# Performance work log

Measured on AMD Instinct MI355X. Metric: run time of the kernel, lower is better.

Reference implementation:

```python
import jax, jax.numpy as jnp
import numpy as np

NUM_CLASSES = 10
MAX_V = 81  # max_width * max_height = 9*9


def _ln(x, w, eps=1e-5):
    # torch LayerNorm with bias=False (weight only)
    m = jnp.mean(x, axis=-1, keepdims=True)
    v = jnp.var(x, axis=-1, keepdims=True)
    return (x - m) / jnp.sqrt(v + eps) * w


def _mha(q_in, k_in, v_in, in_proj, out_proj, nhead):
    # torch nn.MultiheadAttention, bias=False
    d = q_in.shape[-1]
    Wq, Wk, Wv = in_proj[:d], in_proj[d:2 * d], in_proj[2 * d:]
    q = q_in @ Wq.T
    k = k_in @ Wk.T
    v = v_in @ Wv.T
    B, Lq, _ = q.shape
    Lk = k.shape[1]
    hd = d // nhead
    q = q.reshape(B, Lq, nhead, hd)
    k = k.reshape(B, Lk, nhead, hd)
    v = v.reshape(B, Lk, nhead, hd)
    scores = jnp.einsum('bqhd,bkhd->bhqk', q, k) / jnp.sqrt(jnp.asarray(hd, q.dtype))
    attn = jax.nn.softmax(scores, axis=-1)
    o = jnp.einsum('bhqk,bkhd->bqhd', attn, v).reshape(B, Lq, d)
    return o @ out_proj.T


def setup_inputs() -> dict:
    key = jax.random.key(0)
    ks = jax.random.split(key, 16)
    N, C, H, W = 16, NUM_CLASSES, 30, 30
    d = C + 1  # 11
    V = 32

    def rn(k, shape, s=0.2):
        return (jax.random.normal(k, shape) * s).astype(jnp.float32)

    return {
        'x': jax.random.normal(ks[0], (N, C, H, W), dtype=jnp.float32),
        'V_feature': rn(ks[1], (C, V), 1.0),
        'enc_in_proj': rn(ks[2], (3 * d, d)),
        'enc_out_proj': rn(ks[3], (d, d)),
        'enc_lin1': rn(ks[4], (1, d)),
        'enc_lin2': rn(ks[5], (d, 1)),
        'enc_ln1': jnp.ones((d,), jnp.float32),
        'enc_ln2': jnp.ones((d,), jnp.float32),
        'ffV_w': rn(ks[6], (V, MAX_V)),
        'dec_sa_in': rn(ks[7], (3 * V, V)),
        'dec_sa_out': rn(ks[8], (V, V)),
        'dec_ca_in': rn(ks[9], (3 * V, V)),
        'dec_ca_out': rn(ks[10], (V, V)),
        'dec_lin1': rn(ks[11], (1, V)),
        'dec_lin2': rn(ks[12], (V, 1)),
        'dec_ln1': jnp.ones((V,), jnp.float32),
        'dec_ln2': jnp.ones((V,), jnp.float32),
        'dec_ln3': jnp.ones((V,), jnp.float32),
        'W_d0': rn(ks[13], (8, V)),
        'W_d1': rn(ks[14], (1, 8)),
    }


def reference(x, V_feature, enc_in_proj, enc_out_proj, enc_lin1, enc_lin2,
              enc_ln1, enc_ln2, ffV_w, dec_sa_in, dec_sa_out, dec_ca_in,
              dec_ca_out, dec_lin1, dec_lin2, dec_ln1, dec_ln2, dec_ln3,
              W_d0, W_d1):
    N, C, H, W = x.shape
    # PixelVectorExtractor: pad(0) + all-ones channel padded with 1, 3x3 unfold
    xp = jnp.pad(x, ((0, 0), (0, 0), (1, 1), (1, 1)))
    ones = jnp.ones((N, 1, H + 2, W + 2), x.dtype)
    xc = jnp.concatenate([xp, ones], axis=1)  # [N, C+1, H+2, W+2]
    # row-major 3x3 patch order matches torch unfold(0,3,1).unfold(1,3,1)
    patches = jnp.stack([xc[:, :, di:di + H, dj:dj + W]
                         for di in range(3) for dj in range(3)], axis=-1)
    feat = patches.transpose(0, 2, 3, 1, 4).reshape(N * H * W, C + 1, 9)
    feat = jnp.pad(feat, ((0, 0), (0, 0), (0, MAX_V - 9)))  # [B, C+1, 81]

    # TransformerEncoder (1 layer, post-norm, nhead=1, relu FF, no dropout)
    f = feat.transpose(0, 2, 1)  # [B, 81, C+1]
    f = _ln(f + _mha(f, f, f, enc_in_proj, enc_out_proj, 1), enc_ln1)
    f = _ln(f + jax.nn.relu(f @ enc_lin1.T) @ enc_lin2.T, enc_ln2)
    f = f.transpose(0, 2, 1)  # [B, C+1, 81]

    mem = f @ ffV_w.T  # ff_V: Linear(81 -> 32, no bias) -> [B, C+1, 32]
    B, _, V = mem.shape

    # TransformerDecoder (1 layer, post-norm, nhead=32 so head_dim=1)
    y = jnp.broadcast_to(V_feature, (B, C, V))
    y = _ln(y + _mha(y, y, y, dec_sa_in, dec_sa_out, V), dec_ln1)
    y = _ln(y + _mha(y, mem, mem, dec_ca_in, dec_ca_out, V), dec_ln2)
    y = _ln(y + jax.nn.relu(y @ dec_lin1.T) @ dec_lin2.T, dec_ln3)

    # decode MLP: 32 -> 8 -> 1
    y = jax.nn.relu(y @ W_d0.T) @ W_d1.T  # [B, C, 1]
    return y.reshape(N, H, W, C).transpose(0, 3, 1, 2)
```

## Files before the change

### kernel.cpp

```cpp
#include <hip/hip_runtime.h>
#include <math.h>


__device__ __forceinline__ float gsum32(float v) {
#pragma unroll
  for (int m = 16; m > 0; m >>= 1) v += __shfl_xor(v, m, 32);
  return v;
}

__global__ __launch_bounds__(256) void precompute_kernel(
    const float* __restrict__ Vf,
    const float* __restrict__ enc_in,
    const float* __restrict__ enc_outw,
    const float* __restrict__ ffV_w,
    const float* __restrict__ dec_sa_in,
    const float* __restrict__ dec_sa_out,
    const float* __restrict__ dec_ln1,
    const float* __restrict__ dec_ca_in,
    float* __restrict__ M_enc, float* __restrict__ WVO,
    float* __restrict__ G_k, float* __restrict__ G_v,
    float* __restrict__ y1, float* __restrict__ qca)
{
  const int tid = threadIdx.x;
  const float rs11 = 0.3015113445777636f;

  for (int idx = tid; idx < 121; idx += 256) {
    int c = idx / 11, cp = idx - c * 11;
    float sm = 0.f, sv = 0.f;
    for (int i = 0; i < 11; ++i) {
      sm += enc_in[i * 11 + c] * enc_in[(11 + i) * 11 + cp];
      sv += enc_outw[c * 11 + i] * enc_in[(22 + i) * 11 + cp];
    }
    M_enc[idx] = sm * rs11;
    WVO[idx] = sv;
  }

  __shared__ float Fsh[320];
  for (int idx = tid; idx < 288; idx += 256) {
    int t = idx >> 5, j = idx & 31;
    Fsh[idx] = ffV_w[j * 81 + t];
  }
  if (tid < 32) {
    float s = 0.f;
    for (int t = 9; t < 81; ++t) s += ffV_w[tid * 81 + t];
    Fsh[288 + tid] = s;
  }
  __syncthreads();

  for (int idx = tid; idx < 640; idx += 256) {
    int which = idx >= 320;
    int r = idx - 320 * which;
    int t = r >> 5, h = r & 31;
    const float* w = dec_ca_in + ((which ? 64 : 32) + h) * 32;
    float s = 0.f;
    for (int j = 0; j < 32; ++j) s += Fsh[t * 32 + j] * w[j];
    (which ? G_v : G_k)[r] = s;
  }

  __shared__ float qsa[320], ksa[320], vsa[320], osa[320], zb[320];
  __shared__ float mu[16], rstd[16];

  for (int idx = tid; idx < 960; idx += 256) {
    int m = idx / 320, r = idx - m * 320;
    int t = r >> 5, h = r & 31;
    const float* w = dec_sa_in + (m * 32 + h) * 32;
    const float* yr = Vf + t * 32;
    float s = 0.f;
#pragma unroll
    for (int j = 0; j < 32; ++j) s += yr[j] * w[j];
    (m == 0 ? qsa : m == 1 ? ksa : vsa)[r] = s;
  }
  __syncthreads();

  for (int idx = tid; idx < 320; idx += 256) {
    int h = idx & 31;
    float q = qsa[idx];
    float sc[10];
    float mx = -1e30f;
#pragma unroll
    for (int s = 0; s < 10; ++s) { sc[s] = q * ksa[s * 32 + h]; mx = fmaxf(mx, sc[s]); }
    float den = 0.f, acc = 0.f;
#pragma unroll
    for (int s = 0; s < 10; ++s) {
      float e = __expf(sc[s] - mx);
      den += e;
      acc += e * vsa[s * 32 + h];
    }
    osa[idx] = acc / den;
  }
  __syncthreads();

  for (int idx = tid; idx < 320; idx += 256) {
    int t = idx >> 5, c = idx & 31;
    float s = 0.f;
#pragma unroll
    for (int h = 0; h < 32; ++h) s += osa[t * 32 + h] * dec_sa_out[c * 32 + h];
    zb[idx] = Vf[idx] + s;
  }
  __syncthreads();

  if (tid < 10) {
    float s1 = 0.f, s2 = 0.f;
    for (int c = 0; c < 32; ++c) { float z = zb[tid * 32 + c]; s1 += z; s2 += z * z; }
    float m = s1 * (1.f / 32.f);
    mu[tid] = m;
    rstd[tid] = 1.f / sqrtf(s2 * (1.f / 32.f) - m * m + 1e-5f);
  }
  __syncthreads();

  for (int idx = tid; idx < 320; idx += 256) {
    int t = idx >> 5, c = idx & 31;
    float v = (zb[idx] - mu[t]) * rstd[t] * dec_ln1[c];
    y1[idx] = v;
    zb[idx] = v;
  }
  __syncthreads();

  for (int idx = tid; idx < 320; idx += 256) {
    int t = idx >> 5, h = idx & 31;
    const float* w = dec_ca_in + h * 32;
    float s = 0.f;
#pragma unroll
    for (int j = 0; j < 32; ++j) s += zb[t * 32 + j] * w[j];
    qca[idx] = s;
  }
}

#define SLICE 1376

__global__ __launch_bounds__(256) void pixel_main_kernel(
    const float* __restrict__ x,
    const float* __restrict__ M_enc, const float* __restrict__ WVO,
    const float* __restrict__ enc_lin1, const float* __restrict__ enc_lin2,
    const float* __restrict__ enc_ln1, const float* __restrict__ enc_ln2,
    const float* __restrict__ G_k, const float* __restrict__ G_v,
    const float* __restrict__ y1g, const float* __restrict__ qcag,
    const float* __restrict__ dec_ca_out,
    const float* __restrict__ dec_lin1, const float* __restrict__ dec_lin2,
    const float* __restrict__ dec_ln2v, const float* __restrict__ dec_ln3v,
    const float* __restrict__ W_d0, const float* __restrict__ W_d1,
    float* __restrict__ out)
{
  __shared__ __align__(16) float sh[4 * SLICE];
  const int wave = threadIdx.x >> 6;
  const int lane = threadIdx.x & 63;
  float* ls = sh + wave * SLICE;
  const int F9 = 0, G = 112, VO = 224, SC = 336, ZR = 432, FE = 544, KC = 656, VC = 1008;
  const int OC = 0, ZB = 320;

  for (int pp = 0; pp < 2; ++pp) {
    const int p = blockIdx.x * 8 + pp * 4 + wave;
    const int n = p / 900;
    const int rem = p - n * 900;
    const int pi = rem / 30, pj = rem - (rem / 30) * 30;

    for (int idx = lane; idx < 99; idx += 64) {
      int t = idx / 11, c = idx - t * 11;
      float val = 1.0f;
      if (c < 10) {
        int di = t / 3, dj = t - (t / 3) * 3;
        int ii = pi + di - 1, jj = pj + dj - 1;
        val = (ii >= 0 && ii < 30 && jj >= 0 && jj < 30)
                  ? x[((n * 10 + c) * 30 + ii) * 30 + jj] : 0.0f;
      }
      ls[F9 + idx] = val;
    }
    __syncthreads();

    for (int idx = lane; idx < 99; idx += 64) {
      int s = idx / 11, c = idx - (idx / 11) * 11;
      const float* Mr = M_enc + c * 11;
      const float* Wr = WVO + c * 11;
      float ag = 0.f, av = 0.f;
#pragma unroll
      for (int cp = 0; cp < 11; ++cp) {
        float fv = ls[F9 + s * 11 + cp];
        ag += Mr[cp] * fv;
        av += Wr[cp] * fv;
      }
      ls[G + idx] = ag;
      ls[VO + idx] = av;
    }
    __syncthreads();

    for (int idx = lane; idx < 81; idx += 64) {
      int t = idx / 9, s = idx - t * 9;
      float a = 0.f;
#pragma unroll
      for (int c = 0; c < 11; ++c) a += ls[F9 + t * 11 + c] * ls[G + s * 11 + c];
      ls[SC + idx] = a;
    }
    __syncthreads();

    if (lane < 9) {
      float m = 0.f;
#pragma unroll
      for (int s = 0; s < 9; ++s) m = fmaxf(m, ls[SC + lane * 9 + s]);
      ls[FE + lane] = m;
    }
    __syncthreads();

    for (int idx = lane; idx < 81; idx += 64) {
      int t = idx / 9;
      ls[SC + idx] = __expf(ls[SC + idx] - ls[FE + t]);
    }
    __syncthreads();

    if (lane < 9) {
      float den = 72.0f * __expf(-ls[FE + lane]);
#pragma unroll
      for (int s = 0; s < 9; ++s) den += ls[SC + lane * 9 + s];
      ls[FE + 16 + lane] = 1.0f / den;
    }
    __syncthreads();

    for (int idx = lane; idx < 110; idx += 64) {
      int t = idx / 11, c = idx - t * 11;
      float a = 0.f;
      if (t < 9) {
#pragma unroll
        for (int s = 0; s < 9; ++s) a += ls[SC + t * 9 + s] * ls[VO + s * 11 + c];
        a = a * ls[FE + 16 + t] + ls[F9 + idx];
      } else {
#pragma unroll
        for (int s = 0; s < 9; ++s) a += ls[VO + s * 11 + c];
        a *= (1.0f / 81.0f);
      }
      ls[ZR + idx] = a;
    }
    __syncthreads();

    if (lane < 10) {
      float s1 = 0.f, s2 = 0.f;
#pragma unroll
      for (int c = 0; c < 11; ++c) { float z = ls[ZR + lane * 11 + c]; s1 += z; s2 += z * z; }
      float m = s1 * (1.0f / 11.0f);
      ls[SC + lane] = m;
      ls[SC + 16 + lane] = 1.0f / sqrtf(s2 * (1.0f / 11.0f) - m * m + 1e-5f);
    }
    __syncthreads();

    for (int idx = lane; idx < 110; idx += 64) {
      int t = idx / 11, c = idx - t * 11;
      ls[ZR + idx] = (ls[ZR + idx] - ls[SC + t]) * ls[SC + 16 + t] * enc_ln1[c];
    }
    __syncthreads();

    if (lane < 10) {
      float h = 0.f;
#pragma unroll
      for (int c = 0; c < 11; ++c) h += ls[ZR + lane * 11 + c] * enc_lin1[c];
      h = fmaxf(h, 0.f);
      float s1 = 0.f, s2 = 0.f;
#pragma unroll
      for (int c = 0; c < 11; ++c) {
        float z = ls[ZR + lane * 11 + c] + h * enc_lin2[c];
        s1 += z; s2 += z * z;
      }
      float m = s1 * (1.0f / 11.0f);
      ls[SC + 32 + lane] = h;
      ls[SC + 48 + lane] = m;
      ls[SC + 64 + lane] = 1.0f / sqrtf(s2 * (1.0f / 11.0f) - m * m + 1e-5f);
    }
    __syncthreads();

    for (int idx = lane; idx < 110; idx += 64) {
      int t = idx / 11, c = idx - t * 11;
      float z = ls[ZR + idx] + ls[SC + 32 + t] * enc_lin2[c];
      ls[FE + idx] = (z - ls[SC + 48 + t]) * ls[SC + 64 + t] * enc_ln2[c];
    }
    __syncthreads();

    {
      const int h = lane & 31, grp = lane >> 5;
      const float* Gb = grp ? G_v : G_k;
      const int dst = grp ? VC : KC;
      float gr[10];
#pragma unroll
      for (int t = 0; t < 10; ++t) gr[t] = Gb[t * 32 + h];
#pragma unroll
      for (int c = 0; c < 11; ++c) {
        float a = 0.f;
#pragma unroll
        for (int t = 0; t < 10; ++t) a += ls[FE + t * 11 + c] * gr[t];
        ls[dst + c * 32 + h] = a;
      }
    }
    __syncthreads();

    for (int it = 0; it < 5; ++it) {
      int idx = it * 64 + lane;
      int t = idx >> 5, h = idx & 31;
      float q = qcag[t * 32 + h];
      float kreg[11];
#pragma unroll
      for (int s = 0; s < 11; ++s) kreg[s] = q * ls[KC + s * 32 + h];
      float mx = kreg[0];
#pragma unroll
      for (int s = 1; s < 11; ++s) mx = fmaxf(mx, kreg[s]);
      float den = 0.f, acc = 0.f;
#pragma unroll
      for (int s = 0; s < 11; ++s) {
        float e = __expf(kreg[s] - mx);
        den += e;
        acc += e * ls[VC + s * 32 + h];
      }
      ls[OC + idx] = acc / den;
    }
    __syncthreads();

    for (int k = 0; k < 5; ++k) {
      int t = 2 * k + (lane >> 5);
      int c = lane & 31;
      float zacc = 0.f;
      const float4* wrow = (const float4*)(dec_ca_out + c * 32);
      const float4* orow = (const float4*)(ls + OC + t * 32);
#pragma unroll
      for (int h4 = 0; h4 < 8; ++h4) {
        float4 o4 = orow[h4];
        float4 w4 = wrow[h4];
        zacc += o4.x * w4.x + o4.y * w4.y + o4.z * w4.z + o4.w * w4.w;
      }
      float z = y1g[t * 32 + c] + zacc;
      {
        float s1 = gsum32(z), s2 = gsum32(z * z);
        float mu = s1 * (1.0f / 32.0f);
        z = (z - mu) * (1.0f / sqrtf(s2 * (1.0f / 32.0f) - mu * mu + 1e-5f)) * dec_ln2v[c];
      }
      {
        float d1 = gsum32(z * dec_lin1[c]);
        z += fmaxf(d1, 0.f) * dec_lin2[c];
      }
      {
        float s1 = gsum32(z), s2 = gsum32(z * z);
        float mu = s1 * (1.0f / 32.0f);
        z = (z - mu) * (1.0f / sqrtf(s2 * (1.0f / 32.0f) - mu * mu + 1e-5f)) * dec_ln3v[c];
      }
      ls[ZB + t * 32 + c] = z;
    }
    __syncthreads();

    for (int idx = lane; idx < 80; idx += 64) {
      int t = idx >> 3, m = idx & 7;
      const float4* arow = (const float4*)(W_d0 + m * 32);
      const float4* zrow4 = (const float4*)(ls + ZB + t * 32);
      float d = 0.f;
#pragma unroll
      for (int q4 = 0; q4 < 8; ++q4) {
        float4 a4 = arow[q4];
        float4 z4 = zrow4[q4];
        d += a4.x * z4.x + a4.y * z4.y + a4.z * z4.z + a4.w * z4.w;
      }
      ls[OC + idx] = fmaxf(d, 0.f);
    }
    __syncthreads();

    if (lane < 10) {
      float r = 0.f;
#pragma unroll
      for (int m = 0; m < 8; ++m) r += ls[OC + lane * 8 + m] * W_d1[m];
      out[((n * 10 + lane) * 30 + pi) * 30 + pj] = r;
    }
    __syncthreads();
  }
}

extern "C" void kernel_launch(void* const* d_in, const int* in_sizes, int n_in,
                              void* d_out, int out_size, void* d_ws, size_t ws_size,
                              hipStream_t stream) {
  (void)in_sizes; (void)n_in; (void)out_size; (void)ws_size;
  const float* x          = (const float*)d_in[0];
  const float* Vf         = (const float*)d_in[1];
  const float* enc_in     = (const float*)d_in[2];
  const float* enc_outw   = (const float*)d_in[3];
  const float* enc_lin1   = (const float*)d_in[4];
  const float* enc_lin2   = (const float*)d_in[5];
  const float* enc_ln1    = (const float*)d_in[6];
  const float* enc_ln2    = (const float*)d_in[7];
  const float* ffV_w      = (const float*)d_in[8];
  const float* dec_sa_in  = (const float*)d_in[9];
  const float* dec_sa_out = (const float*)d_in[10];
  const float* dec_ca_in  = (const float*)d_in[11];
  const float* dec_ca_out = (const float*)d_in[12];
  const float* dec_lin1   = (const float*)d_in[13];
  const float* dec_lin2   = (const float*)d_in[14];
  const float* dec_ln1    = (const float*)d_in[15];
  const float* dec_ln2    = (const float*)d_in[16];
  const float* dec_ln3    = (const float*)d_in[17];
  const float* W_d0       = (const float*)d_in[18];
  const float* W_d1       = (const float*)d_in[19];
  float* out = (float*)d_out;

  float* ws    = (float*)d_ws;
  float* M_enc = ws;
  float* WVO   = ws + 128;
  float* G_k   = ws + 256;
  float* G_v   = ws + 576;
  float* y1    = ws + 896;
  float* qca   = ws + 1216;

  hipLaunchKernelGGL(precompute_kernel, dim3(1), dim3(256), 0, stream,
                     Vf, enc_in, enc_outw, ffV_w, dec_sa_in, dec_sa_out,
                     dec_ln1, dec_ca_in, M_enc, WVO, G_k, G_v, y1, qca);

  hipLaunchKernelGGL(pixel_main_kernel, dim3(1800), dim3(256), 0, stream,
                     x, M_enc, WVO, enc_lin1, enc_lin2, enc_ln1, enc_ln2,
                     G_k, G_v, y1, qca, dec_ca_out, dec_lin1, dec_lin2,
                     dec_ln2, dec_ln3, W_d0, W_d1, out);
}
```

Measured before the change: 202.6 us.

## Replace block barriers with per-wave LDS waits, split precompute, one pixel per wave

```diff
diff --git a/kernel.cpp b/kernel.cpp
--- a/kernel.cpp
+++ b/kernel.cpp
@@ -6,6 +6,10 @@
 #pragma unroll
   for (int m = 16; m > 0; m >>= 1) v += __shfl_xor(v, m, 32);
   return v;
+}
+
+__device__ __forceinline__ void wsync() {
+  asm volatile("s_waitcnt lgkmcnt(0)" ::: "memory");
 }
 
 __global__ __launch_bounds__(256) void precompute_kernel(
@@ -22,107 +26,109 @@
     float* __restrict__ y1, float* __restrict__ qca)
 {
   const int tid = threadIdx.x;
-  const float rs11 = 0.3015113445777636f;
-
-  for (int idx = tid; idx < 121; idx += 256) {
-    int c = idx / 11, cp = idx - c * 11;
-    float sm = 0.f, sv = 0.f;
-    for (int i = 0; i < 11; ++i) {
-      sm += enc_in[i * 11 + c] * enc_in[(11 + i) * 11 + cp];
-      sv += enc_outw[c * 11 + i] * enc_in[(22 + i) * 11 + cp];
-    }
-    M_enc[idx] = sm * rs11;
-    WVO[idx] = sv;
-  }
-
-  __shared__ float Fsh[320];
-  for (int idx = tid; idx < 288; idx += 256) {
-    int t = idx >> 5, j = idx & 31;
-    Fsh[idx] = ffV_w[j * 81 + t];
-  }
-  if (tid < 32) {
-    float s = 0.f;
-    for (int t = 9; t < 81; ++t) s += ffV_w[tid * 81 + t];
-    Fsh[288 + tid] = s;
-  }
-  __syncthreads();
-
-  for (int idx = tid; idx < 640; idx += 256) {
-    int which = idx >= 320;
-    int r = idx - 320 * which;
-    int t = r >> 5, h = r & 31;
-    const float* w = dec_ca_in + ((which ? 64 : 32) + h) * 32;
-    float s = 0.f;
-    for (int j = 0; j < 32; ++j) s += Fsh[t * 32 + j] * w[j];
-    (which ? G_v : G_k)[r] = s;
-  }
-
-  __shared__ float qsa[320], ksa[320], vsa[320], osa[320], zb[320];
-  __shared__ float mu[16], rstd[16];
-
-  for (int idx = tid; idx < 960; idx += 256) {
-    int m = idx / 320, r = idx - m * 320;
-    int t = r >> 5, h = r & 31;
-    const float* w = dec_sa_in + (m * 32 + h) * 32;
-    const float* yr = Vf + t * 32;
-    float s = 0.f;
-#pragma unroll
-    for (int j = 0; j < 32; ++j) s += yr[j] * w[j];
-    (m == 0 ? qsa : m == 1 ? ksa : vsa)[r] = s;
-  }
-  __syncthreads();
-
-  for (int idx = tid; idx < 320; idx += 256) {
-    int h = idx & 31;
-    float q = qsa[idx];
-    float sc[10];
-    float mx = -1e30f;
-#pragma unroll
-    for (int s = 0; s < 10; ++s) { sc[s] = q * ksa[s * 32 + h]; mx = fmaxf(mx, sc[s]); }
-    float den = 0.f, acc = 0.f;
-#pragma unroll
-    for (int s = 0; s < 10; ++s) {
-      float e = __expf(sc[s] - mx);
-      den += e;
-      acc += e * vsa[s * 32 + h];
-    }
-    osa[idx] = acc / den;
-  }
-  __syncthreads();
-
-  for (int idx = tid; idx < 320; idx += 256) {
-    int t = idx >> 5, c = idx & 31;
-    float s = 0.f;
-#pragma unroll
-    for (int h = 0; h < 32; ++h) s += osa[t * 32 + h] * dec_sa_out[c * 32 + h];
-    zb[idx] = Vf[idx] + s;
-  }
-  __syncthreads();
-
-  if (tid < 10) {
-    float s1 = 0.f, s2 = 0.f;
-    for (int c = 0; c < 32; ++c) { float z = zb[tid * 32 + c]; s1 += z; s2 += z * z; }
-    float m = s1 * (1.f / 32.f);
-    mu[tid] = m;
-    rstd[tid] = 1.f / sqrtf(s2 * (1.f / 32.f) - m * m + 1e-5f);
-  }
-  __syncthreads();
-
-  for (int idx = tid; idx < 320; idx += 256) {
-    int t = idx >> 5, c = idx & 31;
-    float v = (zb[idx] - mu[t]) * rstd[t] * dec_ln1[c];
-    y1[idx] = v;
-    zb[idx] = v;
-  }
-  __syncthreads();
-
-  for (int idx = tid; idx < 320; idx += 256) {
-    int t = idx >> 5, h = idx & 31;
-    const float* w = dec_ca_in + h * 32;
-    float s = 0.f;
-#pragma unroll
-    for (int j = 0; j < 32; ++j) s += zb[t * 32 + j] * w[j];
-    qca[idx] = s;
+
+  if (blockIdx.x == 0) {
+    const float rs11 = 0.3015113445777636f;
+    for (int idx = tid; idx < 121; idx += 256) {
+      int c = idx / 11, cp = idx - c * 11;
+      float sm = 0.f, sv = 0.f;
+      for (int i = 0; i < 11; ++i) {
+        sm += enc_in[i * 11 + c] * enc_in[(11 + i) * 11 + cp];
+        sv += enc_outw[c * 11 + i] * enc_in[(22 + i) * 11 + cp];
+      }
+      M_enc[idx] = sm * rs11;
+      WVO[idx] = sv;
+    }
+
+    __shared__ float Fsh[320];
+    for (int idx = tid; idx < 288; idx += 256) {
+      int t = idx >> 5, j = idx & 31;
+      Fsh[idx] = ffV_w[j * 81 + t];
+    }
+    if (tid < 32) {
+      float s = 0.f;
+      for (int t = 9; t < 81; ++t) s += ffV_w[tid * 81 + t];
+      Fsh[288 + tid] = s;
+    }
+    __syncthreads();
+
+    for (int idx = tid; idx < 640; idx += 256) {
+      int which = idx >= 320;
+      int r = idx - 320 * which;
+      int t = r >> 5, h = r & 31;
+      const float* w = dec_ca_in + ((which ? 64 : 32) + h) * 32;
+      float s = 0.f;
+      for (int j = 0; j < 32; ++j) s += Fsh[t * 32 + j] * w[j];
+      (which ? G_v : G_k)[r] = s;
+    }
+  } else {
+    __shared__ float qsa[320], ksa[320], vsa[320], osa[320], zb[320];
+    __shared__ float mu[16], rstd[16];
+
+    for (int idx = tid; idx < 960; idx += 256) {
+      int m = idx / 320, r = idx - m * 320;
+      int t = r >> 5, h = r & 31;
+      const float* w = dec_sa_in + (m * 32 + h) * 32;
+      const float* yr = Vf + t * 32;
+      float s = 0.f;
+#pragma unroll
+      for (int j = 0; j < 32; ++j) s += yr[j] * w[j];
+      (m == 0 ? qsa : m == 1 ? ksa : vsa)[r] = s;
+    }
+    __syncthreads();
+
+    for (int idx = tid; idx < 320; idx += 256) {
+      int h = idx & 31;
+      float q = qsa[idx];
+      float sc[10];
+      float mx = -1e30f;
+#pragma unroll
+      for (int s = 0; s < 10; ++s) { sc[s] = q * ksa[s * 32 + h]; mx = fmaxf(mx, sc[s]); }
+      float den = 0.f, acc = 0.f;
+#pragma unroll
+      for (int s = 0; s < 10; ++s) {
+        float e = __expf(sc[s] - mx);
+        den += e;
+        acc += e * vsa[s * 32 + h];
+      }
+      osa[idx] = acc / den;
+    }
+    __syncthreads();
+
+    for (int idx = tid; idx < 320; idx += 256) {
+      int t = idx >> 5, c = idx & 31;
+      float s = 0.f;
+#pragma unroll
+      for (int h = 0; h < 32; ++h) s += osa[t * 32 + h] * dec_sa_out[c * 32 + h];
+      zb[idx] = Vf[idx] + s;
+    }
+    __syncthreads();
+
+    if (tid < 10) {
+      float s1 = 0.f, s2 = 0.f;
+      for (int c = 0; c < 32; ++c) { float z = zb[tid * 32 + c]; s1 += z; s2 += z * z; }
+      float m = s1 * (1.f / 32.f);
+      mu[tid] = m;
+      rstd[tid] = 1.f / sqrtf(s2 * (1.f / 32.f) - m * m + 1e-5f);
+    }
+    __syncthreads();
+
+    for (int idx = tid; idx < 320; idx += 256) {
+      int t = idx >> 5, c = idx & 31;
+      float v = (zb[idx] - mu[t]) * rstd[t] * dec_ln1[c];
+      y1[idx] = v;
+      zb[idx] = v;
+    }
+    __syncthreads();
+
+    for (int idx = tid; idx < 320; idx += 256) {
+      int t = idx >> 5, h = idx & 31;
+      const float* w = dec_ca_in + h * 32;
+      float s = 0.f;
+#pragma unroll
+      for (int j = 0; j < 32; ++j) s += zb[t * 32 + j] * w[j];
+      qca[idx] = s;
+    }
   }
 }
 
@@ -148,220 +154,200 @@
   const int F9 = 0, G = 112, VO = 224, SC = 336, ZR = 432, FE = 544, KC = 656, VC = 1008;
   const int OC = 0, ZB = 320;
 
-  for (int pp = 0; pp < 2; ++pp) {
-    const int p = blockIdx.x * 8 + pp * 4 + wave;
-    const int n = p / 900;
-    const int rem = p - n * 900;
-    const int pi = rem / 30, pj = rem - (rem / 30) * 30;
-
-    for (int idx = lane; idx < 99; idx += 64) {
-      int t = idx / 11, c = idx - t * 11;
-      float val = 1.0f;
-      if (c < 10) {
-        int di = t / 3, dj = t - (t / 3) * 3;
-        int ii = pi + di - 1, jj = pj + dj - 1;
-        val = (ii >= 0 && ii < 30 && jj >= 0 && jj < 30)
-                  ? x[((n * 10 + c) * 30 + ii) * 30 + jj] : 0.0f;
-      }
-      ls[F9 + idx] = val;
-    }
-    __syncthreads();
-
-    for (int idx = lane; idx < 99; idx += 64) {
-      int s = idx / 11, c = idx - (idx / 11) * 11;
-      const float* Mr = M_enc + c * 11;
-      const float* Wr = WVO + c * 11;
-      float ag = 0.f, av = 0.f;
-#pragma unroll
-      for (int cp = 0; cp < 11; ++cp) {
-        float fv = ls[F9 + s * 11 + cp];
-        ag += Mr[cp] * fv;
-        av += Wr[cp] * fv;
-      }
-      ls[G + idx] = ag;
-      ls[VO + idx] = av;
-    }
-    __syncthreads();
-
-    for (int idx = lane; idx < 81; idx += 64) {
-      int t = idx / 9, s = idx - t * 9;
+  const int p = blockIdx.x * 4 + wave;
+  const int n = p / 900;
+  const int rem = p - n * 900;
+  const int pi = rem / 30, pj = rem - (rem / 30) * 30;
+
+  for (int idx = lane; idx < 99; idx += 64) {
+    int t = idx / 11, c = idx - t * 11;
+    float val = 1.0f;
+    if (c < 10) {
+      int di = t / 3, dj = t - (t / 3) * 3;
+      int ii = pi + di - 1, jj = pj + dj - 1;
+      val = (ii >= 0 && ii < 30 && jj >= 0 && jj < 30)
+                ? x[((n * 10 + c) * 30 + ii) * 30 + jj] : 0.0f;
+    }
+    ls[F9 + idx] = val;
+  }
+  wsync();
+
+  for (int idx = lane; idx < 99; idx += 64) {
+    int s = idx / 11, c = idx - (idx / 11) * 11;
+    const float* Mr = M_enc + c * 11;
+    const float* Wr = WVO + c * 11;
+    float ag = 0.f, av = 0.f;
+#pragma unroll
+    for (int cp = 0; cp < 11; ++cp) {
+      float fv = ls[F9 + s * 11 + cp];
+      ag += Mr[cp] * fv;
+      av += Wr[cp] * fv;
+    }
+    ls[G + idx] = ag;
+    ls[VO + idx] = av;
+  }
+  wsync();
+
+  for (int idx = lane; idx < 81; idx += 64) {
+    int t = idx / 9, s = idx - (idx / 9) * 9;
+    float a = 0.f;
+#pragma unroll
+    for (int c = 0; c < 11; ++c) a += ls[F9 + t * 11 + c] * ls[G + s * 11 + c];
+    ls[SC + idx] = a;
+  }
+  wsync();
+
+  if (lane < 9) {
+    float e[9];
+    float mx = 0.0f;
+#pragma unroll
+    for (int s = 0; s < 9; ++s) { e[s] = ls[SC + lane * 9 + s]; mx = fmaxf(mx, e[s]); }
+    float den = 72.0f * __expf(-mx);
+#pragma unroll
+    for (int s = 0; s < 9; ++s) {
+      e[s] = __expf(e[s] - mx);
+      den += e[s];
+      ls[SC + lane * 9 + s] = e[s];
+    }
+    ls[SC + 81 + lane] = 1.0f / den;
+  }
+  wsync();
+
+  for (int idx = lane; idx < 110; idx += 64) {
+    int t = idx / 11, c = idx - (idx / 11) * 11;
+    float a = 0.f;
+    if (t < 9) {
+#pragma unroll
+      for (int s = 0; s < 9; ++s) a += ls[SC + t * 9 + s] * ls[VO + s * 11 + c];
+      a = a * ls[SC + 81 + t] + ls[F9 + idx];
+    } else {
+#pragma unroll
+      for (int s = 0; s < 9; ++s) a += ls[VO + s * 11 + c];
+      a *= (1.0f / 81.0f);
+    }
+    ls[ZR + idx] = a;
+  }
+  wsync();
+
+  if (lane < 10) {
+    float row[11];
+#pragma unroll
+    for (int c = 0; c < 11; ++c) row[c] = ls[ZR + lane * 11 + c];
+    float s1 = 0.f, s2 = 0.f;
+#pragma unroll
+    for (int c = 0; c < 11; ++c) { s1 += row[c]; s2 += row[c] * row[c]; }
+    float mu = s1 * (1.0f / 11.0f);
+    float rs = 1.0f / sqrtf(s2 * (1.0f / 11.0f) - mu * mu + 1e-5f);
+    float h = 0.f;
+#pragma unroll
+    for (int c = 0; c < 11; ++c) {
+      row[c] = (row[c] - mu) * rs * enc_ln1[c];
+      h += row[c] * enc_lin1[c];
+    }
+    h = fmaxf(h, 0.f);
+    float t1 = 0.f, t2 = 0.f;
+#pragma unroll
+    for (int c = 0; c < 11; ++c) {
+      row[c] += h * enc_lin2[c];
+      t1 += row[c]; t2 += row[c] * row[c];
+    }
+    float mu2 = t1 * (1.0f / 11.0f);
+    float rs2 = 1.0f / sqrtf(t2 * (1.0f / 11.0f) - mu2 * mu2 + 1e-5f);
+#pragma unroll
+    for (int c = 0; c < 11; ++c)
+      ls[FE + lane * 11 + c] = (row[c] - mu2) * rs2 * enc_ln2[c];
+  }
+  wsync();
+
+  {
+    const int h = lane & 31, grp = lane >> 5;
+    const float* Gb = grp ? G_v : G_k;
+    const int dst = grp ? VC : KC;
+    float gr[10];
+#pragma unroll
+    for (int t = 0; t < 10; ++t) gr[t] = Gb[t * 32 + h];
+#pragma unroll
+    for (int c = 0; c < 11; ++c) {
       float a = 0.f;
 #pragma unroll
-      for (int c = 0; c < 11; ++c) a += ls[F9 + t * 11 + c] * ls[G + s * 11 + c];
-      ls[SC + idx] = a;
-    }
-    __syncthreads();
-
-    if (lane < 9) {
-      float m = 0.f;
-#pragma unroll
-      for (int s = 0; s < 9; ++s) m = fmaxf(m, ls[SC + lane * 9 + s]);
-      ls[FE + lane] = m;
-    }
-    __syncthreads();
-
-    for (int idx = lane; idx < 81; idx += 64) {
-      int t = idx / 9;
-      ls[SC + idx] = __expf(ls[SC + idx] - ls[FE + t]);
-    }
-    __syncthreads();
-
-    if (lane < 9) {
-      float den = 72.0f * __expf(-ls[FE + lane]);
-#pragma unroll
-      for (int s = 0; s < 9; ++s) den += ls[SC + lane * 9 + s];
-      ls[FE + 16 + lane] = 1.0f / den;
-    }
-    __syncthreads();
-
-    for (int idx = lane; idx < 110; idx += 64) {
-      int t = idx / 11, c = idx - t * 11;
-      float a = 0.f;
-      if (t < 9) {
-#pragma unroll
-        for (int s = 0; s < 9; ++s) a += ls[SC + t * 9 + s] * ls[VO + s * 11 + c];
-        a = a * ls[FE + 16 + t] + ls[F9 + idx];
-      } else {
-#pragma unroll
-        for (int s = 0; s < 9; ++s) a += ls[VO + s * 11 + c];
-        a *= (1.0f / 81.0f);
-      }
-      ls[ZR + idx] = a;
-    }
-    __syncthreads();
-
-    if (lane < 10) {
-      float s1 = 0.f, s2 = 0.f;
-#pragma unroll
-      for (int c = 0; c < 11; ++c) { float z = ls[ZR + lane * 11 + c]; s1 += z; s2 += z * z; }
-      float m = s1 * (1.0f / 11.0f);
-      ls[SC + lane] = m;
-      ls[SC + 16 + lane] = 1.0f / sqrtf(s2 * (1.0f / 11.0f) - m * m + 1e-5f);
-    }
-    __syncthreads();
-
-    for (int idx = lane; idx < 110; idx += 64) {
-      int t = idx / 11, c = idx - t * 11;
-      ls[ZR + idx] = (ls[ZR + idx] - ls[SC + t]) * ls[SC + 16 + t] * enc_ln1[c];
-    }
-    __syncthreads();
-
-    if (lane < 10) {
-      float h = 0.f;
-#pragma unroll
-      for (int c = 0; c < 11; ++c) h += ls[ZR + lane * 11 + c] * enc_lin1[c];
-      h = fmaxf(h, 0.f);
-      float s1 = 0.f, s2 = 0.f;
-#pragma unroll
-      for (int c = 0; c < 11; ++c) {
-        float z = ls[ZR + lane * 11 + c] + h * enc_lin2[c];
-        s1 += z; s2 += z * z;
-      }
-      float m = s1 * (1.0f / 11.0f);
-      ls[SC + 32 + lane] = h;
-      ls[SC + 48 + lane] = m;
-      ls[SC + 64 + lane] = 1.0f / sqrtf(s2 * (1.0f / 11.0f) - m * m + 1e-5f);
-    }
-    __syncthreads();
-
-    for (int idx = lane; idx < 110; idx += 64) {
-      int t = idx / 11, c = idx - t * 11;
-      float z = ls[ZR + idx] + ls[SC + 32 + t] * enc_lin2[c];
-      ls[FE + idx] = (z - ls[SC + 48 + t]) * ls[SC + 64 + t] * enc_ln2[c];
-    }
-    __syncthreads();
-
+      for (int t = 0; t < 10; ++t) a += ls[FE + t * 11 + c] * gr[t];
+      ls[dst + c * 32 + h] = a;
+    }
+  }
+  wsync();
+
+  for (int it = 0; it < 5; ++it) {
+    int idx = it * 64 + lane;
+    int t = idx >> 5, h = idx & 31;
+    float q = qcag[t * 32 + h];
+    float kreg[11];
+#pragma unroll
+    for (int s = 0; s < 11; ++s) kreg[s] = q * ls[KC + s * 32 + h];
+    float mx = kreg[0];
+#pragma unroll
+    for (int s = 1; s < 11; ++s) mx = fmaxf(mx, kreg[s]);
+    float den = 0.f, acc = 0.f;
+#pragma unroll
+    for (int s = 0; s < 11; ++s) {
+      float e = __expf(kreg[s] - mx);
+      den += e;
+      acc += e * ls[VC + s * 32 + h];
+    }
+    ls[OC + idx] = acc / den;
+  }
+  wsync();
+
+  for (int k = 0; k < 5; ++k) {
+    int t = 2 * k + (lane >> 5);
+    int c = lane & 31;
+    float zacc = 0.f;
+    const float4* wrow = (const float4*)(dec_ca_out + c * 32);
+    const float4* orow = (const float4*)(ls + OC + t * 32);
+#pragma unroll
+    for (int h4 = 0; h4 < 8; ++h4) {
+      float4 o4 = orow[h4];
+      float4 w4 = wrow[h4];
+      zacc += o4.x * w4.x + o4.y * w4.y + o4.z * w4.z + o4.w * w4.w;
+    }
+    float z = y1g[t * 32 + c] + zacc;
     {
-      const int h = lane & 31, grp = lane >> 5;
-      const float* Gb = grp ? G_v : G_k;
-      const int dst = grp ? VC : KC;
-      float gr[10];
-#pragma unroll
-      for (int t = 0; t < 10; ++t) gr[t] = Gb[t * 32 + h];
-#pragma unroll
-      for (int c = 0; c < 11; ++c) {
-        float a = 0.f;
-#pragma unroll
-        for (int t = 0; t < 10; ++t) a += ls[FE + t * 11 + c] * gr[t];
-        ls[dst + c * 32 + h] = a;
-      }
-    }
-    __syncthreads();
-
-    for (int it = 0; it < 5; ++it) {
-      int idx = it * 64 + lane;
-      int t = idx >> 5, h = idx & 31;
-      float q = qcag[t * 32 + h];
-      float kreg[11];
-#pragma unroll
-      for (int s = 0; s < 11; ++s) kreg[s] = q * ls[KC + s * 32 + h];
-      float mx = kreg[0];
-#pragma unroll
-      for (int s = 1; s < 11; ++s) mx = fmaxf(mx, kreg[s]);
-      float den = 0.f, acc = 0.f;
-#pragma unroll
-      for (int s = 0; s < 11; ++s) {
-        float e = __expf(kreg[s] - mx);
-        den += e;
-        acc += e * ls[VC + s * 32 + h];
-      }
-      ls[OC + idx] = acc / den;
-    }
-    __syncthreads();
-
-    for (int k = 0; k < 5; ++k) {
-      int t = 2 * k + (lane >> 5);
-      int c = lane & 31;
-      float zacc = 0.f;
-      const float4* wrow = (const float4*)(dec_ca_out + c * 32);
-      const float4* orow = (const float4*)(ls + OC + t * 32);
-#pragma unroll
-      for (int h4 = 0; h4 < 8; ++h4) {
-        float4 o4 = orow[h4];
-        float4 w4 = wrow[h4];
-        zacc += o4.x * w4.x + o4.y * w4.y + o4.z * w4.z + o4.w * w4.w;
-      }
-      float z = y1g[t * 32 + c] + zacc;
-      {
-        float s1 = gsum32(z), s2 = gsum32(z * z);
-        float mu = s1 * (1.0f / 32.0f);
-        z = (z - mu) * (1.0f / sqrtf(s2 * (1.0f / 32.0f) - mu * mu + 1e-5f)) * dec_ln2v[c];
-      }
-      {
-        float d1 = gsum32(z * dec_lin1[c]);
-        z += fmaxf(d1, 0.f) * dec_lin2[c];
-      }
-      {
-        float s1 = gsum32(z), s2 = gsum32(z * z);
-        float mu = s1 * (1.0f / 32.0f);
-        z = (z - mu) * (1.0f / sqrtf(s2 * (1.0f / 32.0f) - mu * mu + 1e-5f)) * dec_ln3v[c];
-      }
-      ls[ZB + t * 32 + c] = z;
-    }
-    __syncthreads();
-
-    for (int idx = lane; idx < 80; idx += 64) {
-      int t = idx >> 3, m = idx & 7;
-      const float4* arow = (const float4*)(W_d0 + m * 32);
-      const float4* zrow4 = (const float4*)(ls + ZB + t * 32);
-      float d = 0.f;
-#pragma unroll
-      for (int q4 = 0; q4 < 8; ++q4) {
-        float4 a4 = arow[q4];
-        float4 z4 = zrow4[q4];
-        d += a4.x * z4.x + a4.y * z4.y + a4.z * z4.z + a4.w * z4.w;
-      }
-      ls[OC + idx] = fmaxf(d, 0.f);
-    }
-    __syncthreads();
-
-    if (lane < 10) {
-      float r = 0.f;
-#pragma unroll
-      for (int m = 0; m < 8; ++m) r += ls[OC + lane * 8 + m] * W_d1[m];
-      out[((n * 10 + lane) * 30 + pi) * 30 + pj] = r;
-    }
-    __syncthreads();
+      float s1 = gsum32(z), s2 = gsum32(z * z);
+      float mu = s1 * (1.0f / 32.0f);
+      z = (z - mu) * (1.0f / sqrtf(s2 * (1.0f / 32.0f) - mu * mu + 1e-5f)) * dec_ln2v[c];
+    }
+    {
+      float d1 = gsum32(z * dec_lin1[c]);
+      z += fmaxf(d1, 0.f) * dec_lin2[c];
+    }
+    {
+      float s1 = gsum32(z), s2 = gsum32(z * z);
+      float mu = s1 * (1.0f / 32.0f);
+      z = (z - mu) * (1.0f / sqrtf(s2 * (1.0f / 32.0f) - mu * mu + 1e-5f)) * dec_ln3v[c];
+    }
+    ls[ZB + t * 32 + c] = z;
+  }
+  wsync();
+
+  for (int idx = lane; idx < 80; idx += 64) {
+    int t = idx >> 3, m = idx & 7;
+    const float4* arow = (const float4*)(W_d0 + m * 32);
+    const float4* zrow4 = (const float4*)(ls + ZB + t * 32);
+    float d = 0.f;
+#pragma unroll
+    for (int q4 = 0; q4 < 8; ++q4) {
+      float4 a4 = arow[q4];
+      float4 z4 = zrow4[q4];
+      d += a4.x * z4.x + a4.y * z4.y + a4.z * z4.z + a4.w * z4.w;
+    }
+    ls[OC + idx] = fmaxf(d, 0.f);
+  }
+  wsync();
+
+  if (lane < 10) {
+    float r = 0.f;
+#pragma unroll
+    for (int m = 0; m < 8; ++m) r += ls[OC + lane * 8 + m] * W_d1[m];
+    out[((n * 10 + lane) * 30 + pi) * 30 + pj] = r;
   }
 }
 
@@ -399,11 +385,11 @@
   float* y1    = ws + 896;
   float* qca   = ws + 1216;
 
-  hipLaunchKernelGGL(precompute_kernel, dim3(1), dim3(256), 0, stream,
+  hipLaunchKernelGGL(precompute_kernel, dim3(2), dim3(256), 0, stream,
                      Vf, enc_in, enc_outw, ffV_w, dec_sa_in, dec_sa_out,
                      dec_ln1, dec_ca_in, M_enc, WVO, G_k, G_v, y1, qca);
 
-  hipLaunchKernelGGL(pixel_main_kernel, dim3(1800), dim3(256), 0, stream,
+  hipLaunchKernelGGL(pixel_main_kernel, dim3(3600), dim3(256), 0, stream,
                      x, M_enc, WVO, enc_lin1, enc_lin2, enc_ln1, enc_ln2,
                      G_k, G_v, y1, qca, dec_ca_out, dec_lin1, dec_lin2,
                      dec_ln2, dec_ln3, W_d0, W_d1, out);
```

After: 171.5 us. -15.3%, faster.
